# Kernel optimization log

Measured on AMD Instinct MI355X. Metric: run time of the kernel, lower is better.

## Reference

```python
import jax, jax.numpy as jnp
import numpy as np
from jax import lax

B, W, H, C = 32, 512, 512, 3
PSF = 32


def setup_inputs() -> dict:
    key = jax.random.key(0)
    k1, k2, k3 = jax.random.split(key, 3)
    observed_images = jax.random.normal(k1, (B, W, H, C), dtype=jnp.float32)
    # trainable vars of the keras model (estimated_image would be initialized to
    # mean(observed) on the first call; we treat it as a free parameter)
    estimated_image = jax.random.normal(k2, (W, H, C), dtype=jnp.float32)
    point_spread_functions = jax.random.normal(k3, (B, PSF, PSF, 1, C), dtype=jnp.float32) * 0.05
    return {
        "observed_images": observed_images,
        "estimated_image": estimated_image,
        "point_spread_functions": point_spread_functions,
    }


def _per_example_conv(img_nhwc, psf_hwio):
    # img_nhwc: [1, W, H, C]; psf_hwio: [k, k, 1, C] -> grouped (depthwise) conv,
    # feature_group_count = C, matching tf.nn.conv2d's grouped-conv semantics.
    out = lax.conv_general_dilated(
        img_nhwc, psf_hwio,
        window_strides=(1, 1), padding="SAME",
        dimension_numbers=("NHWC", "HWIO", "NHWC"),
        feature_group_count=img_nhwc.shape[-1],
    )
    return out[0]  # [W, H, C]


def reference(observed_images, estimated_image, point_spread_functions):
    img = estimated_image[None]  # [1, W, H, C], shared across batch
    # vmap over the per-example PSF kernels replaces the python loop of B conv2d calls
    predicted = jax.vmap(lambda psf: _per_example_conv(img, psf))(point_spread_functions)
    # predicted: [B, W, H, C]
    loss = jnp.mean((observed_images - predicted) ** 2)
    return predicted, loss
```

## Files before the change

### kernel.cpp

```cpp
#include <hip/hip_runtime.h>
#include <hip/hip_bf16.h>

#define BATCH 32
#define WDIM 512
#define HDIM 512
#define CDIM 3
#define KPSF 32
#define NPRED (BATCH*WDIM*HDIM*CDIM)

#define TW 88
#define TH 63
#define TE (TW*TH)
#define TALL (TW*TH*CDIM)

typedef __bf16 bf16x8 __attribute__((ext_vector_type(8)));
typedef float floatx16 __attribute__((ext_vector_type(16)));
typedef float fx4 __attribute__((ext_vector_type(4)));

__device__ __forceinline__ void barrier_lgkm() {
    __asm__ volatile("s_waitcnt lgkmcnt(0)\n\ts_barrier" ::: "memory");
}

__global__ __launch_bounds__(64) void pack_psf(const float* __restrict__ psf,
                                               __bf16* __restrict__ dst,
                                               float* __restrict__ loss) {
    if (blockIdx.x == 0 && threadIdx.x == 0) *loss = 0.f;
    int idx = blockIdx.x;
    int h = idx & 1;
    int j = (idx >> 1) & 31;
    int c = idx >> 6;
    int lane = threadIdx.x;
    int b = lane & 31;
    int q = lane >> 5;
    bf16x8 v;
#pragma unroll
    for (int t = 0; t < 8; ++t) {
        int i = 16*h + 8*q + t;
        v[t] = (__bf16)psf[((size_t)(b*KPSF + i)*KPSF + j)*CDIM + c];
    }
    *(bf16x8*)(dst + (size_t)(idx*64 + lane)*8) = v;
}

__global__ __launch_bounds__(192, 2) void conv_mfma(
    const float* __restrict__ obs,
    const float* __restrict__ img,
    const __bf16* __restrict__ psfA,
    float* __restrict__ out)
{
    __shared__ __align__(16) unsigned char smem[CDIM*TE*2];
    __bf16 (*sImg)[TE] = (__bf16 (*)[TE])smem;
    float* sOut = (float*)smem;

    const int tid  = threadIdx.x;
    const int lane = tid & 63;
    const int c    = tid >> 6;
    const int n    = lane & 31;
    const int q    = lane >> 5;

    const int bx = blockIdx.x;
    const int r8 = bx & 7;
    const int g  = (bx >> 3) & 7;
    const int yt = bx >> 6;
    const int x0 = g*64 + r8;
    const int ytile = yt*32;

    const bool interior = (x0 >= 15) && (x0 <= WDIM - 73) &&
                          (ytile >= 15) && (ytile <= HDIM - 48);
    if (interior) {
        const int col0 = (ytile - 15)*3;
        const int p2 = col0 & 3;
        const float* gb = img + (size_t)(x0 - 15)*(HDIM*CDIM) + (col0 - p2);
#pragma unroll 2
        for (int f = tid; f < 88*48; f += 192) {
            int r = f / 48;
            int v = f - r*48;
            fx4 val = *(const fx4*)(gb + (size_t)r*(HDIM*CDIM) + 4*v);
            int d = 4*v - p2;
#pragma unroll
            for (int u = 0; u < 4; ++u) {
                int dd = d + u;
                if (dd >= 0 && dd < 189) {
                    int yl = (dd*171) >> 9;
                    int cc = dd - 3*yl;
                    sImg[cc][yl*TW + r] = (__bf16)val[u];
                }
            }
        }
    } else {
#pragma unroll 4
        for (int e = tid; e < TALL; e += 192) {
            int xl = e / (TH*CDIM);
            int rr = e - xl*(TH*CDIM);
            int yl = rr / 3;
            int cc = rr - yl*3;
            int xg = x0 + xl - 15;
            int yg = ytile + yl - 15;
            float v = 0.f;
            if ((unsigned)xg < WDIM && (unsigned)yg < HDIM)
                v = img[((size_t)xg*HDIM + yg)*CDIM + cc];
            sImg[cc][yl*TW + xl] = (__bf16)v;
        }
    }
    __syncthreads();

    floatx16 acc[8] = {};
    const __bf16* pA = psfA + (size_t)c*(KPSF*2*64*8) + (size_t)lane*8;
    const __bf16* sI = (const __bf16*)&sImg[c][q*8];

    bf16x8 A0 = *(const bf16x8*)(pA);
    bf16x8 A1 = *(const bf16x8*)(pA + 512);
#pragma unroll 4
    for (int j = 0; j < 32; ++j) {
        bf16x8 cA0 = A0, cA1 = A1;
        if (j < 31) {
            A0 = *(const bf16x8*)(pA + (size_t)(j+1)*1024);
            A1 = *(const bf16x8*)(pA + (size_t)(j+1)*1024 + 512);
        }
        const __bf16* rowp = sI + (n + j)*TW;
        bf16x8 C[10];
#pragma unroll
        for (int rr = 0; rr < 10; ++rr)
            C[rr] = *(const bf16x8*)(rowp + rr*8);
#pragma unroll
        for (int s = 0; s < 8; ++s) {
            acc[s] = __builtin_amdgcn_mfma_f32_32x32x16_bf16(cA0, C[s],   acc[s], 0, 0, 0);
            acc[s] = __builtin_amdgcn_mfma_f32_32x32x16_bf16(cA1, C[s+2], acc[s], 0, 0, 0);
        }
    }

    float ls = 0.f;
    size_t base[4];
#pragma unroll
    for (int k = 0; k < 4; ++k) {
        int f = tid + 192*k;
        int fb = f / 24;
        int rem = (f - fb*24) * 4;
        base[k] = (((size_t)fb*WDIM + x0)*HDIM + ytile)*CDIM + rem;
    }
    fx4 obA[4], obB[4];
#pragma unroll
    for (int k = 0; k < 4; ++k)
        obA[k] = __builtin_nontemporal_load((const fx4*)&obs[base[k]]);
#pragma unroll
    for (int k = 0; k < 4; ++k)
        obB[k] = __builtin_nontemporal_load((const fx4*)&obs[base[k] + 8*HDIM*CDIM]);

#pragma unroll 1
    for (int s = 0; s < 8; ++s) {
        barrier_lgkm();
#pragma unroll
        for (int rr = 0; rr < 16; ++rr) {
            int b = (rr & 3) + 8*(rr >> 2) + 4*q;
            sOut[(b*32 + n)*3 + c] = acc[s][rr];
        }
        barrier_lgkm();
        fx4 cur[4];
#pragma unroll
        for (int k = 0; k < 4; ++k) { cur[k] = obA[k]; obA[k] = obB[k]; }
        if (s < 6) {
#pragma unroll
            for (int k = 0; k < 4; ++k)
                obB[k] = __builtin_nontemporal_load(
                    (const fx4*)&obs[base[k] + (size_t)(s+2)*8*HDIM*CDIM]);
        }
#pragma unroll
        for (int k = 0; k < 4; ++k) {
            fx4 p = *(const fx4*)&sOut[4*(tid + 192*k)];
            __builtin_nontemporal_store(p, (fx4*)&out[base[k] + (size_t)s*8*HDIM*CDIM]);
            fx4 d = cur[k] - p;
            ls += d[0]*d[0] + d[1]*d[1] + d[2]*d[2] + d[3]*d[3];
        }
    }

#pragma unroll
    for (int m = 32; m >= 1; m >>= 1) ls += __shfl_xor(ls, m, 64);
    if (lane == 0) atomicAdd(out + NPRED, ls * (1.0f/(float)NPRED));
}

extern "C" void kernel_launch(void* const* d_in, const int* in_sizes, int n_in,
                              void* d_out, int out_size, void* d_ws, size_t ws_size,
                              hipStream_t stream) {
    const float* obs = (const float*)d_in[0];
    const float* img = (const float*)d_in[1];
    const float* psf = (const float*)d_in[2];
    float* out = (float*)d_out;
    __bf16* psfA = (__bf16*)d_ws;

    pack_psf<<<192, 64, 0, stream>>>(psf, psfA, out + NPRED);
    conv_mfma<<<1024, 192, 0, stream>>>(obs, img, psfA, out);
}
```

Baseline: 263.1 us.

## Split conv MFMA into two half passes interleaved with epilogue stores

The 8-accumulator MFMA loop becomes two passes of 4 accumulators each. Each pass's output is written out, with the loss computed, before the second pass's compute starts, and blocks alternate which half they do first so memory traffic overlaps other blocks' compute. Separate LDS buffers for the image and the output tile plus a smaller register footprint allow raising the occupancy hint from 2 to 3 blocks per CU. The cost is reloading the PSF A-fragments twice from global memory without prefetch, and extra LDS use.

```diff
diff --git a/kernel.cpp b/kernel.cpp
--- a/kernel.cpp
+++ b/kernel.cpp
@@ -41,15 +41,14 @@
     *(bf16x8*)(dst + (size_t)(idx*64 + lane)*8) = v;
 }
 
-__global__ __launch_bounds__(192, 2) void conv_mfma(
+__global__ __launch_bounds__(192, 3) void conv_mfma(
     const float* __restrict__ obs,
     const float* __restrict__ img,
     const __bf16* __restrict__ psfA,
     float* __restrict__ out)
 {
-    __shared__ __align__(16) unsigned char smem[CDIM*TE*2];
-    __bf16 (*sImg)[TE] = (__bf16 (*)[TE])smem;
-    float* sOut = (float*)smem;
+    __shared__ __align__(16) __bf16 sImg[CDIM][TE];
+    __shared__ __align__(16) float sOut[32*32*3];
 
     const int tid  = threadIdx.x;
     const int lane = tid & 63;
@@ -63,6 +62,7 @@
     const int yt = bx >> 6;
     const int x0 = g*64 + r8;
     const int ytile = yt*32;
+    const int g0 = bx & 1;
 
     const bool interior = (x0 >= 15) && (x0 <= WDIM - 73) &&
                           (ytile >= 15) && (ytile <= HDIM - 48);
@@ -103,30 +103,8 @@
     }
     __syncthreads();
 
-    floatx16 acc[8] = {};
     const __bf16* pA = psfA + (size_t)c*(KPSF*2*64*8) + (size_t)lane*8;
     const __bf16* sI = (const __bf16*)&sImg[c][q*8];
-
-    bf16x8 A0 = *(const bf16x8*)(pA);
-    bf16x8 A1 = *(const bf16x8*)(pA + 512);
-#pragma unroll 4
-    for (int j = 0; j < 32; ++j) {
-        bf16x8 cA0 = A0, cA1 = A1;
-        if (j < 31) {
-            A0 = *(const bf16x8*)(pA + (size_t)(j+1)*1024);
-            A1 = *(const bf16x8*)(pA + (size_t)(j+1)*1024 + 512);
-        }
-        const __bf16* rowp = sI + (n + j)*TW;
-        bf16x8 C[10];
-#pragma unroll
-        for (int rr = 0; rr < 10; ++rr)
-            C[rr] = *(const bf16x8*)(rowp + rr*8);
-#pragma unroll
-        for (int s = 0; s < 8; ++s) {
-            acc[s] = __builtin_amdgcn_mfma_f32_32x32x16_bf16(cA0, C[s],   acc[s], 0, 0, 0);
-            acc[s] = __builtin_amdgcn_mfma_f32_32x32x16_bf16(cA1, C[s+2], acc[s], 0, 0, 0);
-        }
-    }
 
     float ls = 0.f;
     size_t base[4];
@@ -140,35 +118,66 @@
     fx4 obA[4], obB[4];
 #pragma unroll
     for (int k = 0; k < 4; ++k)
-        obA[k] = __builtin_nontemporal_load((const fx4*)&obs[base[k]]);
+        obA[k] = __builtin_nontemporal_load(
+            (const fx4*)&obs[base[k] + (size_t)(4*g0 + 0)*12288]);
 #pragma unroll
     for (int k = 0; k < 4; ++k)
-        obB[k] = __builtin_nontemporal_load((const fx4*)&obs[base[k] + 8*HDIM*CDIM]);
+        obB[k] = __builtin_nontemporal_load(
+            (const fx4*)&obs[base[k] + (size_t)(4*g0 + 1)*12288]);
 
 #pragma unroll 1
-    for (int s = 0; s < 8; ++s) {
-        barrier_lgkm();
-#pragma unroll
-        for (int rr = 0; rr < 16; ++rr) {
-            int b = (rr & 3) + 8*(rr >> 2) + 4*q;
-            sOut[(b*32 + n)*3 + c] = acc[s][rr];
-        }
-        barrier_lgkm();
-        fx4 cur[4];
-#pragma unroll
-        for (int k = 0; k < 4; ++k) { cur[k] = obA[k]; obA[k] = obB[k]; }
-        if (s < 6) {
-#pragma unroll
-            for (int k = 0; k < 4; ++k)
-                obB[k] = __builtin_nontemporal_load(
-                    (const fx4*)&obs[base[k] + (size_t)(s+2)*8*HDIM*CDIM]);
-        }
-#pragma unroll
+    for (int p = 0; p < 2; ++p) {
+        const int grp = p ^ g0;
+        const int s0  = 4*grp;
+
+        floatx16 acc[4] = {};
+        const __bf16* sIs = sI + s0*8;
+#pragma unroll 4
+        for (int j = 0; j < 32; ++j) {
+            bf16x8 A0 = *(const bf16x8*)(pA + (size_t)j*1024);
+            bf16x8 A1 = *(const bf16x8*)(pA + (size_t)j*1024 + 512);
+            const __bf16* rowp = sIs + (n + j)*TW;
+            bf16x8 C[6];
+#pragma unroll
+            for (int rr = 0; rr < 6; ++rr)
+                C[rr] = *(const bf16x8*)(rowp + rr*8);
+#pragma unroll
+            for (int ss = 0; ss < 4; ++ss) {
+                acc[ss] = __builtin_amdgcn_mfma_f32_32x32x16_bf16(A0, C[ss],   acc[ss], 0, 0, 0);
+                acc[ss] = __builtin_amdgcn_mfma_f32_32x32x16_bf16(A1, C[ss+2], acc[ss], 0, 0, 0);
+            }
+        }
+
+#pragma unroll 1
         for (int k = 0; k < 4; ++k) {
-            fx4 p = *(const fx4*)&sOut[4*(tid + 192*k)];
-            __builtin_nontemporal_store(p, (fx4*)&out[base[k] + (size_t)s*8*HDIM*CDIM]);
-            fx4 d = cur[k] - p;
-            ls += d[0]*d[0] + d[1]*d[1] + d[2]*d[2] + d[3]*d[3];
+            const int s = s0 + k;
+            const int t = 4*p + k;
+            barrier_lgkm();
+#pragma unroll
+            for (int rr = 0; rr < 16; ++rr) {
+                int b = (rr & 3) + 8*(rr >> 2) + 4*q;
+                sOut[(b*32 + n)*3 + c] = acc[k][rr];
+            }
+            barrier_lgkm();
+            fx4 cur[4];
+#pragma unroll
+            for (int kk = 0; kk < 4; ++kk) { cur[kk] = obA[kk]; obA[kk] = obB[kk]; }
+            if (t <= 5) {
+                const int tn = t + 2;
+                const int sn = 4*((tn >> 2) ^ g0) + (tn & 3);
+#pragma unroll
+                for (int kk = 0; kk < 4; ++kk)
+                    obB[kk] = __builtin_nontemporal_load(
+                        (const fx4*)&obs[base[kk] + (size_t)sn*12288]);
+            }
+#pragma unroll
+            for (int kk = 0; kk < 4; ++kk) {
+                fx4 pv = *(const fx4*)&sOut[4*(tid + 192*kk)];
+                __builtin_nontemporal_store(pv,
+                    (fx4*)&out[base[kk] + (size_t)s*12288]);
+                fx4 d = cur[kk] - pv;
+                ls += d[0]*d[0] + d[1]*d[1] + d[2]*d[2] + d[3]*d[3];
+            }
         }
     }
 
```

Result: slower. 303.9 us (+15.5%).
